# Kernel optimization log

Measured on AMD Instinct MI355X. Metric: run time of the kernel, lower is better.

Reference implementation:

```python
import jax, jax.numpy as jnp
import numpy as np

B, S, I, H, C, V = 512, 64, 300, 1024, 2, 50000


def setup_inputs() -> dict:
    key = jax.random.key(0)
    ks = jax.random.split(key, 10)
    s = 0.05
    return {
        "x": jax.random.randint(ks[0], (B, S), 0, V),
        "lengths": jax.random.randint(ks[1], (B,), 1, S + 1),
        "embed": jax.random.normal(ks[2], (V, I), jnp.float32) * s,
        "Wih_e": jax.random.normal(ks[3], (4 * H, I), jnp.float32) * s,
        "Whh_e": jax.random.normal(ks[4], (4 * H, H), jnp.float32) * s,
        "bih_e": jnp.zeros((4 * H,), jnp.float32),
        "bhh_e": jnp.zeros((4 * H,), jnp.float32),
        "Wih_d": jax.random.normal(ks[5], (4 * H, I), jnp.float32) * s,
        "Whh_d": jax.random.normal(ks[6], (4 * H, H), jnp.float32) * s,
        "bih_d": jnp.zeros((4 * H,), jnp.float32),
        "bhh_d": jnp.zeros((4 * H,), jnp.float32),
        "W_lin": jax.random.normal(ks[7], (C, H), jnp.float32) * s,
        "b_lin": jnp.zeros((C,), jnp.float32),
    }


def lstm_cell(xi, h, c, Wih, Whh, bih, bhh):
    # PyTorch LSTMCell gate order: i, f, g, o
    g = xi @ Wih.T + bih + h @ Whh.T + bhh
    i, f, gg, o = jnp.split(g, 4, axis=-1)
    c = jax.nn.sigmoid(f) * c + jax.nn.sigmoid(i) * jnp.tanh(gg)
    return jax.nn.sigmoid(o) * jnp.tanh(c), c


def reference(x, lengths, embed, Wih_e, Whh_e, bih_e, bhh_e,
              Wih_d, Whh_d, bih_d, bhh_d, W_lin, b_lin):
    bsz, slen = x.shape
    hdim = Whh_e.shape[1]
    ncls = W_lin.shape[0]
    xs = embed[x.T]                      # [S, B, I] (seq-major, like x.transpose(0,1))

    h0 = jnp.zeros((bsz, hdim), xs.dtype)
    c0 = jnp.zeros((bsz, hdim), xs.dtype)

    def enc_step(carry, xi):
        h, c = carry
        h, c = lstm_cell(xi, h, c, Wih_e, Whh_e, bih_e, bhh_e)
        return (h, c), h

    # forward pass over sequence
    (h, c), enc_fwd = jax.lax.scan(enc_step, (h0, c0), xs)          # enc_fwd: [S,B,H]
    # backward pass with the SAME encoder cell, continuing from (h, c)
    (h, c), h_bwd = jax.lax.scan(enc_step, (h, c), xs[::-1])        # h_bwd:  [S,B,H]
    # k-th backward step pairs with encoder_forward[k] in the original code
    enc_out = (enc_fwd + h_bwd) * 0.5                               # [S,B,H]

    def dec_step(carry, xi):
        h, c = carry
        # original attention sums over batch AND hidden -> one scalar per timestep,
        # and rebuilds w as a fresh Variable (no gradient through the weights).
        w = jax.nn.softmax(jnp.sum(h[None, :, :] * enc_out, axis=(1, 2)))  # [S]
        w = jax.lax.stop_gradient(w)
        h = h + jnp.einsum('t,tbh->bh', w, enc_out)
        h, c = lstm_cell(xi, h, c, Wih_d, Whh_d, bih_d, bhh_d)
        return (h, c), h

    _, dec = jax.lax.scan(dec_step, (h, c), xs)                     # [S,B,H]

    out = dec @ W_lin.T + b_lin                                     # [S,B,C]
    out = out.transpose(1, 0, 2)                                    # [B,S,C]
    pad = jnp.array([1.0, 0.0], out.dtype)                          # overwrite beyond lengths
    mask = jnp.arange(slen)[None, :] < lengths[:, None]             # [B,S]
    out = jnp.where(mask[:, :, None], out, pad)
    return out.reshape(bsz * slen, ncls)
```

## Files before the change

### kernel.cpp

```cpp
#include <hip/hip_runtime.h>
#include <hip/hip_bf16.h>

#define BSZ 512
#define SEQ 64
#define IDIM 300
#define KP1 384
#define HDIM 1024
#define G4 4096
#define BH (BSZ*HDIM)

typedef __attribute__((ext_vector_type(8))) short bf16x8;
typedef __attribute__((ext_vector_type(4))) float f32x4;
typedef __attribute__((ext_vector_type(8))) unsigned short u16x8;
typedef __attribute__((ext_vector_type(4))) unsigned short u16x4;

__device__ __forceinline__ float sigmoidf_(float x){ return 1.f/(1.f+__expf(-x)); }
__device__ __forceinline__ float bf2f(unsigned short u){
    union{unsigned int i; float f;} v; v.i = ((unsigned)u)<<16; return v.f;
}
__device__ __forceinline__ unsigned short f2bf(float f){
    __hip_bfloat16 b = __float2bfloat16(f);
    return *(unsigned short*)&b;
}

__global__ void embed_gather_k(const int* __restrict__ x, const float* __restrict__ embed,
                               __hip_bfloat16* __restrict__ xs){
    int t = blockIdx.x, b = blockIdx.y;
    int ix = x[b*SEQ + t];
    const float* src = embed + (size_t)ix * IDIM;
    __hip_bfloat16* dst = xs + ((size_t)t*BSZ + b) * KP1;
    for (int k = threadIdx.x; k < KP1; k += 64)
        dst[k] = __float2bfloat16(k < IDIM ? src[k] : 0.f);
}

__global__ void conv_w_k(const float* __restrict__ Wih_e, const float* __restrict__ Wih_d,
                         const float* __restrict__ Whh_e, const float* __restrict__ Whh_d,
                         __hip_bfloat16* __restrict__ Pe, __hip_bfloat16* __restrict__ Pd,
                         __hip_bfloat16* __restrict__ He, __hip_bfloat16* __restrict__ Hd){
    int nr = blockIdx.x, v = blockIdx.y;
    int orig = ((nr>>5)&3)*HDIM + (nr>>7)*32 + (nr&31);
    if (v < 2){
        const float* src = (v ? Wih_d : Wih_e) + (size_t)orig*IDIM;
        __hip_bfloat16* dst = (v ? Pd : Pe) + (size_t)nr*KP1;
        for (int k = threadIdx.x; k < KP1; k += 64)
            dst[k] = __float2bfloat16(k < IDIM ? src[k] : 0.f);
    } else {
        const float* src = ((v == 3) ? Whh_d : Whh_e) + (size_t)orig*HDIM;
        __hip_bfloat16* dst = ((v == 3) ? Hd : He) + (size_t)nr*HDIM;
        for (int k = threadIdx.x; k < HDIM; k += 64)
            dst[k] = __float2bfloat16(src[k]);
    }
}

__global__ void bias_comb_k(const float* __restrict__ a, const float* __restrict__ b2,
                            const float* __restrict__ c2, const float* __restrict__ d2,
                            float* __restrict__ be, float* __restrict__ bd){
    int i = blockIdx.x*256 + threadIdx.x;
    int nr = i & 4095;
    int orig = ((nr>>5)&3)*HDIM + (nr>>7)*32 + (nr&31);
    if (i < G4) be[nr] = a[orig] + b2[orig];
    else        bd[nr] = c2[orig] + d2[orig];
}

__global__ void zero_hc_k(float* __restrict__ h, float* __restrict__ c,
                          __hip_bfloat16* __restrict__ h_bf){
    int idx = blockIdx.x*256 + threadIdx.x;
    h[idx] = 0.f; c[idx] = 0.f; h_bf[idx] = __float2bfloat16(0.f);
}

#define BM 64
#define BN 128
#define NK1 (KP1/128)
#define NK2 (HDIM/128)
#define NKT (NK1+NK2)

__global__ __launch_bounds__(512) void lstm_step_k(
    const __hip_bfloat16* __restrict__ A1, const __hip_bfloat16* __restrict__ B1,
    const __hip_bfloat16* __restrict__ A2, const __hip_bfloat16* __restrict__ B2,
    const float* __restrict__ bias,
    float* __restrict__ c, float* __restrict__ h, __hip_bfloat16* __restrict__ h_bf,
    __hip_bfloat16* __restrict__ encSlot, int mode)
{
    __shared__ __align__(16) char smem[98304];
    const int tid  = threadIdx.x;
    const int lane = tid & 63, wv = tid >> 6;
    const int row0 = blockIdx.y * BM;
    const int col0 = blockIdx.x * BN;
    const int wm = wv >> 2, wn = wv & 3;

    f32x4 acc[2][2] = {};

    auto stage = [&](int ks, int p){
        const __hip_bfloat16* A; const __hip_bfloat16* B; int KA, k0;
        if (ks < NK1){ A = A1; B = B1; KA = KP1;  k0 = ks*128; }
        else         { A = A2; B = B2; KA = HDIM; k0 = (ks-NK1)*128; }
        char* base = smem + p*49152;
        #pragma unroll
        for (int half = 0; half < 2; ++half){
            int u = half*512 + tid;
            int r = u >> 4, s = u & 15;
            int g = s ^ (r & 15);
            const __hip_bfloat16* src = A + (size_t)(row0 + r)*KA + k0 + g*8;
            char* dst = base + half*8192 + wv*1024;
            __builtin_amdgcn_global_load_lds(
                (const __attribute__((address_space(1))) void*)src,
                (__attribute__((address_space(3))) void*)dst, 16, 0, 0);
        }
        #pragma unroll
        for (int q = 0; q < 4; ++q){
            int u = q*512 + tid;
            int r = u >> 4, s = u & 15;
            int g = s ^ (r & 15);
            const __hip_bfloat16* src = B + (size_t)(col0 + r)*KA + k0 + g*8;
            char* dst = base + 16384 + q*8192 + wv*1024;
            __builtin_amdgcn_global_load_lds(
                (const __attribute__((address_space(1))) void*)src,
                (__attribute__((address_space(3))) void*)dst, 16, 0, 0);
        }
    };

    auto compute = [&](int p){
        const char* Ab = smem + p*49152;
        const char* Bb = Ab + 16384;
        const int rr = lane & 15, g = lane >> 4;
        bf16x8 af[2][4], bfr[2][4];
        #pragma unroll
        for (int m = 0; m < 2; ++m){
            int r = wm*32 + m*16 + rr;
            #pragma unroll
            for (int kk = 0; kk < 4; ++kk)
                af[m][kk] = *(const bf16x8*)(Ab + r*256 + ((kk*4 + g) ^ (r & 15))*16);
        }
        #pragma unroll
        for (int n = 0; n < 2; ++n){
            int r = wn*32 + n*16 + rr;
            #pragma unroll
            for (int kk = 0; kk < 4; ++kk)
                bfr[n][kk] = *(const bf16x8*)(Bb + r*256 + ((kk*4 + g) ^ (r & 15))*16);
        }
        #pragma unroll
        for (int kk = 0; kk < 4; ++kk)
            #pragma unroll
            for (int m = 0; m < 2; ++m)
                #pragma unroll
                for (int n = 0; n < 2; ++n)
                    acc[m][n] = __builtin_amdgcn_mfma_f32_16x16x32_bf16(af[m][kk], bfr[n][kk], acc[m][n], 0, 0, 0);
    };

    const int erow = tid >> 3;
    const int ejj0 = (tid & 7) * 4;
    const size_t ebase = (size_t)(row0 + erow)*HDIM + blockIdx.x*32 + ejj0;

    stage(0, 0);
    const f32x4 cpre = *(const f32x4*)(c + ebase);
    __syncthreads();
    for (int ks = 0; ks < NKT; ++ks){
        int p = ks & 1;
        if (ks + 1 < NKT) stage(ks + 1, p ^ 1);
        compute(p);
        __syncthreads();
    }

    float* ep = (float*)smem;
    {
        const int rr = lane & 15, q4 = lane >> 4;
        #pragma unroll
        for (int m = 0; m < 2; ++m){
            int row = wm*32 + m*16 + q4*4;
            #pragma unroll
            for (int n = 0; n < 2; ++n){
                int jj = n*16 + rr;
                float bi = bias[col0 + wn*32 + jj];
                #pragma unroll
                for (int q = 0; q < 4; ++q)
                    ep[(wn*64 + row + q)*33 + jj] = acc[m][n][q] + bi;
            }
        }
    }
    __syncthreads();
    {
        f32x4 cv, hv;
        #pragma unroll
        for (int e = 0; e < 4; ++e){
            float gi = ep[(0*64 + erow)*33 + ejj0 + e];
            float gf = ep[(1*64 + erow)*33 + ejj0 + e];
            float gg = ep[(2*64 + erow)*33 + ejj0 + e];
            float go = ep[(3*64 + erow)*33 + ejj0 + e];
            float cc = sigmoidf_(gf)*cpre[e] + sigmoidf_(gi)*tanhf(gg);
            float hh = sigmoidf_(go)*tanhf(cc);
            cv[e] = cc; hv[e] = hh;
        }
        *(f32x4*)(c + ebase) = cv;
        *(f32x4*)(h + ebase) = hv;
        u16x4 hb;
        #pragma unroll
        for (int e = 0; e < 4; ++e) hb[e] = f2bf(hv[e]);
        *(u16x4*)(h_bf + ebase) = hb;
        if (mode == 0){
            *(u16x4*)(encSlot + ebase) = hb;
        } else if (mode == 1){
            u16x4 eo = *(const u16x4*)(encSlot + ebase);
            u16x4 r;
            #pragma unroll
            for (int e = 0; e < 4; ++e) r[e] = f2bf(0.5f*(bf2f(eo[e]) + hv[e]));
            *(u16x4*)(encSlot + ebase) = r;
        }
    }
}

__global__ __launch_bounds__(256) void attn_part_k(
    const __hip_bfloat16* __restrict__ h_bf, const __hip_bfloat16* __restrict__ enc,
    float* __restrict__ part,
    const float* __restrict__ h, const float* __restrict__ Wl, const float* __restrict__ bl,
    const int* __restrict__ len, float* __restrict__ out, int dect)
{
    __shared__ float red[4];
    int lane = threadIdx.x & 63, w = threadIdx.x >> 6;
    if (blockIdx.x < 64){
        int ch = blockIdx.x;
        int s  = blockIdx.y;
        const u16x8* e  = (const u16x8*)(enc + (size_t)s*BH + (size_t)ch*8192);
        const u16x8* hp = (const u16x8*)(h_bf + (size_t)ch*8192);
        float sum = 0.f;
        for (int i = threadIdx.x; i < 1024; i += 256){
            u16x8 ev = e[i], hv = hp[i];
            #pragma unroll
            for (int j = 0; j < 8; ++j) sum += bf2f(hv[j]) * bf2f(ev[j]);
        }
        #pragma unroll
        for (int m = 32; m >= 1; m >>= 1) sum += __shfl_xor(sum, m);
        if (lane == 0) red[w] = sum;
        __syncthreads();
        if (threadIdx.x == 0) part[s*64 + ch] = red[0]+red[1]+red[2]+red[3];
    } else if (dect >= 0){
        int b = ((blockIdx.x - 64)*64 + blockIdx.y)*4 + w;
        const float* hb = h + (size_t)b*HDIM;
        float s0 = 0.f, s1 = 0.f;
        for (int j = lane; j < HDIM; j += 64){
            float v = hb[j];
            s0 += v * Wl[j];
            s1 += v * Wl[HDIM + j];
        }
        #pragma unroll
        for (int m = 32; m >= 1; m >>= 1){ s0 += __shfl_xor(s0, m); s1 += __shfl_xor(s1, m); }
        if (lane == 0){
            bool valid = dect < len[b];
            size_t r = ((size_t)b*SEQ + dect)*2;
            out[r]   = valid ? (s0 + bl[0]) : 1.0f;
            out[r+1] = valid ? (s1 + bl[1]) : 0.0f;
        }
    }
}

__global__ __launch_bounds__(256) void attn_apply_k(
    const float* __restrict__ h, const float* __restrict__ part,
    const __hip_bfloat16* __restrict__ enc, __hip_bfloat16* __restrict__ hat_bf)
{
    __shared__ float wl[64];
    int lane = threadIdx.x & 63;
    if (threadIdx.x < 64){
        float tot = 0.f;
        #pragma unroll 8
        for (int ch = 0; ch < 64; ++ch) tot += part[lane*64 + ch];
        float m = tot;
        #pragma unroll
        for (int msk = 32; msk >= 1; msk >>= 1) m = fmaxf(m, __shfl_xor(m, msk));
        float e = __expf(tot - m);
        float sm = e;
        #pragma unroll
        for (int msk = 32; msk >= 1; msk >>= 1) sm += __shfl_xor(sm, msk);
        wl[lane] = e / sm;
    }
    __syncthreads();
    size_t i4 = ((size_t)blockIdx.x*256 + threadIdx.x) * 4;
    float v[4];
    {
        f32x4 a = *(const f32x4*)(h + i4);
        v[0]=a[0]; v[1]=a[1]; v[2]=a[2]; v[3]=a[3];
    }
    for (int s = 0; s < SEQ; ++s){
        u16x4 ev = *(const u16x4*)(enc + (size_t)s*BH + i4);
        float w = wl[s];
        #pragma unroll
        for (int j = 0; j < 4; ++j) v[j] += w * bf2f(ev[j]);
    }
    u16x4 ov;
    #pragma unroll
    for (int j = 0; j < 4; ++j) ov[j] = f2bf(v[j]);
    *(u16x4*)(hat_bf + i4) = ov;
}

__global__ void dec_linear_k(const float* __restrict__ h, const float* __restrict__ Wl,
                             const float* __restrict__ bl, const int* __restrict__ len,
                             float* __restrict__ out, int t)
{
    int b = blockIdx.x, lane = threadIdx.x;
    const float* hb = h + (size_t)b*HDIM;
    float s0 = 0.f, s1 = 0.f;
    for (int j = lane; j < HDIM; j += 64){
        float v = hb[j];
        s0 += v * Wl[j];
        s1 += v * Wl[HDIM + j];
    }
    #pragma unroll
    for (int m = 32; m >= 1; m >>= 1){ s0 += __shfl_xor(s0, m); s1 += __shfl_xor(s1, m); }
    if (lane == 0){
        bool valid = t < len[b];
        size_t r = ((size_t)b*SEQ + t)*2;
        out[r]   = valid ? (s0 + bl[0]) : 1.0f;
        out[r+1] = valid ? (s1 + bl[1]) : 0.0f;
    }
}

extern "C" void kernel_launch(void* const* d_in, const int* in_sizes, int n_in,
                              void* d_out, int out_size, void* d_ws, size_t ws_size,
                              hipStream_t stream)
{
    (void)in_sizes; (void)n_in; (void)out_size; (void)ws_size;
    const int*   x      = (const int*)  d_in[0];
    const int*   len    = (const int*)  d_in[1];
    const float* embed  = (const float*)d_in[2];
    const float* Wih_e  = (const float*)d_in[3];
    const float* Whh_e  = (const float*)d_in[4];
    const float* bih_e  = (const float*)d_in[5];
    const float* bhh_e  = (const float*)d_in[6];
    const float* Wih_d  = (const float*)d_in[7];
    const float* Whh_d  = (const float*)d_in[8];
    const float* bih_d  = (const float*)d_in[9];
    const float* bhh_d  = (const float*)d_in[10];
    const float* W_lin  = (const float*)d_in[11];
    const float* b_lin  = (const float*)d_in[12];
    float* out = (float*)d_out;

    float* ws = (float*)d_ws;
    size_t off = 0;
    auto alloc = [&](size_t nfloats){ size_t o = off; off += (nfloats + 63) & ~(size_t)63; return o; };
    __hip_bfloat16* xs_bf  = (__hip_bfloat16*)(ws + alloc((size_t)SEQ*BSZ*KP1/2));
    __hip_bfloat16* Pe     = (__hip_bfloat16*)(ws + alloc((size_t)G4*KP1/2));
    __hip_bfloat16* Pd     = (__hip_bfloat16*)(ws + alloc((size_t)G4*KP1/2));
    __hip_bfloat16* He     = (__hip_bfloat16*)(ws + alloc((size_t)G4*HDIM/2));
    __hip_bfloat16* Hd     = (__hip_bfloat16*)(ws + alloc((size_t)G4*HDIM/2));
    float* be   = ws + alloc(G4);
    float* bd   = ws + alloc(G4);
    float* h    = ws + alloc(BH);
    float* c    = ws + alloc(BH);
    __hip_bfloat16* h_bf   = (__hip_bfloat16*)(ws + alloc(BH/2));
    __hip_bfloat16* hat_bf = (__hip_bfloat16*)(ws + alloc(BH/2));
    __hip_bfloat16* enc    = (__hip_bfloat16*)(ws + alloc((size_t)SEQ*BH/2));
    float* part = ws + alloc(64*64);

    embed_gather_k<<<dim3(SEQ, BSZ), 64, 0, stream>>>(x, embed, xs_bf);
    conv_w_k<<<dim3(G4, 4), 64, 0, stream>>>(Wih_e, Wih_d, Whh_e, Whh_d, Pe, Pd, He, Hd);
    bias_comb_k<<<32, 256, 0, stream>>>(bih_e, bhh_e, bih_d, bhh_d, be, bd);
    zero_hc_k<<<BH/256, 256, 0, stream>>>(h, c, h_bf);

    dim3 ggrid(G4/BN, BSZ/BM);

    for (int t = 0; t < SEQ; ++t)
        lstm_step_k<<<ggrid, 512, 0, stream>>>(xs_bf + (size_t)t*BSZ*KP1, Pe, h_bf, He, be,
                                               c, h, h_bf, enc + (size_t)t*BH, 0);
    for (int k = 0; k < SEQ; ++k)
        lstm_step_k<<<ggrid, 512, 0, stream>>>(xs_bf + (size_t)(SEQ-1-k)*BSZ*KP1, Pe, h_bf, He, be,
                                               c, h, h_bf, enc + (size_t)k*BH, 1);
    for (int t = 0; t < SEQ; ++t){
        attn_part_k<<<dim3(66, 64), 256, 0, stream>>>(h_bf, enc, part, h, W_lin, b_lin, len, out, t - 1);
        attn_apply_k<<<512, 256, 0, stream>>>(h, part, enc, hat_bf);
        lstm_step_k<<<ggrid, 512, 0, stream>>>(xs_bf + (size_t)t*BSZ*KP1, Pd, hat_bf, Hd, bd,
                                               c, h, h_bf, nullptr, 2);
    }
    dec_linear_k<<<BSZ, 64, 0, stream>>>(h, W_lin, b_lin, len, out, SEQ - 1);
}
```

Baseline: 4.348 ms.

## Use 4-wave LSTM GEMM blocks with larger per-wave tiles and batch attention scores

The LSTM step GEMM now runs 256 threads (4 waves) per block instead of 512, and each wave computes a 32x64 output tile with 8 MFMA accumulators. This raises fragment reuse per LDS read but halves the waves available for latency hiding. The gate epilogue is remapped so each thread handles 8 contiguous columns with wider vector stores. Separately, the attention score kernel keeps h in registers and reuses it across 8 timesteps per block, which cuts repeated h loads and shrinks the grid from 66x64 to 640 blocks.

```diff
diff --git a/kernel.cpp b/kernel.cpp
--- a/kernel.cpp
+++ b/kernel.cpp
@@ -74,7 +74,7 @@
 #define NK2 (HDIM/128)
 #define NKT (NK1+NK2)
 
-__global__ __launch_bounds__(512) void lstm_step_k(
+__global__ __launch_bounds__(256) void lstm_step_k(
     const __hip_bfloat16* __restrict__ A1, const __hip_bfloat16* __restrict__ B1,
     const __hip_bfloat16* __restrict__ A2, const __hip_bfloat16* __restrict__ B2,
     const float* __restrict__ bias,
@@ -86,9 +86,9 @@
     const int lane = tid & 63, wv = tid >> 6;
     const int row0 = blockIdx.y * BM;
     const int col0 = blockIdx.x * BN;
-    const int wm = wv >> 2, wn = wv & 3;
-
-    f32x4 acc[2][2] = {};
+    const int wm = wv >> 1, wn = wv & 1;
+
+    f32x4 acc[2][4] = {};
 
     auto stage = [&](int ks, int p){
         const __hip_bfloat16* A; const __hip_bfloat16* B; int KA, k0;
@@ -96,23 +96,23 @@
         else         { A = A2; B = B2; KA = HDIM; k0 = (ks-NK1)*128; }
         char* base = smem + p*49152;
         #pragma unroll
-        for (int half = 0; half < 2; ++half){
-            int u = half*512 + tid;
+        for (int q = 0; q < 4; ++q){
+            int u = q*256 + tid;
             int r = u >> 4, s = u & 15;
             int g = s ^ (r & 15);
             const __hip_bfloat16* src = A + (size_t)(row0 + r)*KA + k0 + g*8;
-            char* dst = base + half*8192 + wv*1024;
+            char* dst = base + q*4096 + wv*1024;
             __builtin_amdgcn_global_load_lds(
                 (const __attribute__((address_space(1))) void*)src,
                 (__attribute__((address_space(3))) void*)dst, 16, 0, 0);
         }
         #pragma unroll
-        for (int q = 0; q < 4; ++q){
-            int u = q*512 + tid;
+        for (int q = 0; q < 8; ++q){
+            int u = q*256 + tid;
             int r = u >> 4, s = u & 15;
             int g = s ^ (r & 15);
             const __hip_bfloat16* src = B + (size_t)(col0 + r)*KA + k0 + g*8;
-            char* dst = base + 16384 + q*8192 + wv*1024;
+            char* dst = base + 16384 + q*4096 + wv*1024;
             __builtin_amdgcn_global_load_lds(
                 (const __attribute__((address_space(1))) void*)src,
                 (__attribute__((address_space(3))) void*)dst, 16, 0, 0);
@@ -123,7 +123,7 @@
         const char* Ab = smem + p*49152;
         const char* Bb = Ab + 16384;
         const int rr = lane & 15, g = lane >> 4;
-        bf16x8 af[2][4], bfr[2][4];
+        bf16x8 af[2][4], bfr[4][4];
         #pragma unroll
         for (int m = 0; m < 2; ++m){
             int r = wm*32 + m*16 + rr;
@@ -132,8 +132,8 @@
                 af[m][kk] = *(const bf16x8*)(Ab + r*256 + ((kk*4 + g) ^ (r & 15))*16);
         }
         #pragma unroll
-        for (int n = 0; n < 2; ++n){
-            int r = wn*32 + n*16 + rr;
+        for (int n = 0; n < 4; ++n){
+            int r = wn*64 + n*16 + rr;
             #pragma unroll
             for (int kk = 0; kk < 4; ++kk)
                 bfr[n][kk] = *(const bf16x8*)(Bb + r*256 + ((kk*4 + g) ^ (r & 15))*16);
@@ -143,16 +143,17 @@
             #pragma unroll
             for (int m = 0; m < 2; ++m)
                 #pragma unroll
-                for (int n = 0; n < 2; ++n)
+                for (int n = 0; n < 4; ++n)
                     acc[m][n] = __builtin_amdgcn_mfma_f32_16x16x32_bf16(af[m][kk], bfr[n][kk], acc[m][n], 0, 0, 0);
     };
 
-    const int erow = tid >> 3;
-    const int ejj0 = (tid & 7) * 4;
+    const int erow = tid >> 2;
+    const int ejj0 = (tid & 3) * 8;
     const size_t ebase = (size_t)(row0 + erow)*HDIM + blockIdx.x*32 + ejj0;
 
     stage(0, 0);
-    const f32x4 cpre = *(const f32x4*)(c + ebase);
+    const f32x4 cpre0 = *(const f32x4*)(c + ebase);
+    const f32x4 cpre1 = *(const f32x4*)(c + ebase + 4);
     __syncthreads();
     for (int ks = 0; ks < NKT; ++ks){
         int p = ks & 1;
@@ -168,42 +169,46 @@
         for (int m = 0; m < 2; ++m){
             int row = wm*32 + m*16 + q4*4;
             #pragma unroll
-            for (int n = 0; n < 2; ++n){
-                int jj = n*16 + rr;
-                float bi = bias[col0 + wn*32 + jj];
+            for (int n = 0; n < 4; ++n){
+                int cib = wn*64 + n*16 + rr;
+                int gate = cib >> 5, jj = cib & 31;
+                float bi = bias[col0 + cib];
                 #pragma unroll
                 for (int q = 0; q < 4; ++q)
-                    ep[(wn*64 + row + q)*33 + jj] = acc[m][n][q] + bi;
+                    ep[(gate*64 + row + q)*33 + jj] = acc[m][n][q] + bi;
             }
         }
     }
     __syncthreads();
     {
-        f32x4 cv, hv;
-        #pragma unroll
-        for (int e = 0; e < 4; ++e){
+        f32x4 cv0, cv1, hv0, hv1;
+        float hvf[8];
+        #pragma unroll
+        for (int e = 0; e < 8; ++e){
             float gi = ep[(0*64 + erow)*33 + ejj0 + e];
             float gf = ep[(1*64 + erow)*33 + ejj0 + e];
             float gg = ep[(2*64 + erow)*33 + ejj0 + e];
             float go = ep[(3*64 + erow)*33 + ejj0 + e];
-            float cc = sigmoidf_(gf)*cpre[e] + sigmoidf_(gi)*tanhf(gg);
+            float cp = (e < 4) ? cpre0[e] : cpre1[e-4];
+            float cc = sigmoidf_(gf)*cp + sigmoidf_(gi)*tanhf(gg);
             float hh = sigmoidf_(go)*tanhf(cc);
-            cv[e] = cc; hv[e] = hh;
-        }
-        *(f32x4*)(c + ebase) = cv;
-        *(f32x4*)(h + ebase) = hv;
-        u16x4 hb;
-        #pragma unroll
-        for (int e = 0; e < 4; ++e) hb[e] = f2bf(hv[e]);
-        *(u16x4*)(h_bf + ebase) = hb;
+            if (e < 4){ cv0[e] = cc; hv0[e] = hh; } else { cv1[e-4] = cc; hv1[e-4] = hh; }
+            hvf[e] = hh;
+        }
+        *(f32x4*)(c + ebase) = cv0; *(f32x4*)(c + ebase + 4) = cv1;
+        *(f32x4*)(h + ebase) = hv0; *(f32x4*)(h + ebase + 4) = hv1;
+        u16x8 hb;
+        #pragma unroll
+        for (int e = 0; e < 8; ++e) hb[e] = f2bf(hvf[e]);
+        *(u16x8*)(h_bf + ebase) = hb;
         if (mode == 0){
-            *(u16x4*)(encSlot + ebase) = hb;
+            *(u16x8*)(encSlot + ebase) = hb;
         } else if (mode == 1){
-            u16x4 eo = *(const u16x4*)(encSlot + ebase);
-            u16x4 r;
-            #pragma unroll
-            for (int e = 0; e < 4; ++e) r[e] = f2bf(0.5f*(bf2f(eo[e]) + hv[e]));
-            *(u16x4*)(encSlot + ebase) = r;
+            u16x8 eo = *(const u16x8*)(encSlot + ebase);
+            u16x8 r;
+            #pragma unroll
+            for (int e = 0; e < 8; ++e) r[e] = f2bf(0.5f*(bf2f(eo[e]) + hvf[e]));
+            *(u16x8*)(encSlot + ebase) = r;
         }
     }
 }
@@ -214,26 +219,39 @@
     const float* __restrict__ h, const float* __restrict__ Wl, const float* __restrict__ bl,
     const int* __restrict__ len, float* __restrict__ out, int dect)
 {
-    __shared__ float red[4];
     int lane = threadIdx.x & 63, w = threadIdx.x >> 6;
-    if (blockIdx.x < 64){
-        int ch = blockIdx.x;
-        int s  = blockIdx.y;
-        const u16x8* e  = (const u16x8*)(enc + (size_t)s*BH + (size_t)ch*8192);
+    if (blockIdx.x < 512){
+        int ch = blockIdx.x & 63;
+        int s0 = (blockIdx.x >> 6) * 8;
         const u16x8* hp = (const u16x8*)(h_bf + (size_t)ch*8192);
-        float sum = 0.f;
-        for (int i = threadIdx.x; i < 1024; i += 256){
-            u16x8 ev = e[i], hv = hp[i];
-            #pragma unroll
-            for (int j = 0; j < 8; ++j) sum += bf2f(hv[j]) * bf2f(ev[j]);
-        }
-        #pragma unroll
-        for (int m = 32; m >= 1; m >>= 1) sum += __shfl_xor(sum, m);
-        if (lane == 0) red[w] = sum;
+        float hf[4][8];
+        #pragma unroll
+        for (int k = 0; k < 4; ++k){
+            u16x8 hv = hp[threadIdx.x + k*256];
+            #pragma unroll
+            for (int j = 0; j < 8; ++j) hf[k][j] = bf2f(hv[j]);
+        }
+        __shared__ float red[8][4];
+        for (int si = 0; si < 8; ++si){
+            const u16x8* e = (const u16x8*)(enc + (size_t)(s0 + si)*BH + (size_t)ch*8192);
+            float sum = 0.f;
+            #pragma unroll
+            for (int k = 0; k < 4; ++k){
+                u16x8 ev = e[threadIdx.x + k*256];
+                #pragma unroll
+                for (int j = 0; j < 8; ++j) sum += hf[k][j] * bf2f(ev[j]);
+            }
+            #pragma unroll
+            for (int m = 32; m >= 1; m >>= 1) sum += __shfl_xor(sum, m);
+            if (lane == 0) red[si][w] = sum;
+        }
         __syncthreads();
-        if (threadIdx.x == 0) part[s*64 + ch] = red[0]+red[1]+red[2]+red[3];
+        if (threadIdx.x < 8){
+            int si = threadIdx.x;
+            part[(s0 + si)*64 + ch] = red[si][0]+red[si][1]+red[si][2]+red[si][3];
+        }
     } else if (dect >= 0){
-        int b = ((blockIdx.x - 64)*64 + blockIdx.y)*4 + w;
+        int b = (blockIdx.x - 512)*4 + w;
         const float* hb = h + (size_t)b*HDIM;
         float s0 = 0.f, s1 = 0.f;
         for (int j = lane; j < HDIM; j += 64){
@@ -357,15 +375,15 @@
     dim3 ggrid(G4/BN, BSZ/BM);
 
     for (int t = 0; t < SEQ; ++t)
-        lstm_step_k<<<ggrid, 512, 0, stream>>>(xs_bf + (size_t)t*BSZ*KP1, Pe, h_bf, He, be,
+        lstm_step_k<<<ggrid, 256, 0, stream>>>(xs_bf + (size_t)t*BSZ*KP1, Pe, h_bf, He, be,
                                                c, h, h_bf, enc + (size_t)t*BH, 0);
     for (int k = 0; k < SEQ; ++k)
-        lstm_step_k<<<ggrid, 512, 0, stream>>>(xs_bf + (size_t)(SEQ-1-k)*BSZ*KP1, Pe, h_bf, He, be,
+        lstm_step_k<<<ggrid, 256, 0, stream>>>(xs_bf + (size_t)(SEQ-1-k)*BSZ*KP1, Pe, h_bf, He, be,
                                                c, h, h_bf, enc + (size_t)k*BH, 1);
     for (int t = 0; t < SEQ; ++t){
-        attn_part_k<<<dim3(66, 64), 256, 0, stream>>>(h_bf, enc, part, h, W_lin, b_lin, len, out, t - 1);
+        attn_part_k<<<640, 256, 0, stream>>>(h_bf, enc, part, h, W_lin, b_lin, len, out, t - 1);
         attn_apply_k<<<512, 256, 0, stream>>>(h, part, enc, hat_bf);
-        lstm_step_k<<<ggrid, 512, 0, stream>>>(xs_bf + (size_t)t*BSZ*KP1, Pd, hat_bf, Hd, bd,
+        lstm_step_k<<<ggrid, 256, 0, stream>>>(xs_bf + (size_t)t*BSZ*KP1, Pd, hat_bf, Hd, bd,
                                                c, h, h_bf, nullptr, 2);
     }
     dec_linear_k<<<BSZ, 64, 0, stream>>>(h, W_lin, b_lin, len, out, SEQ - 1);
```

After: 4.394 ms. No clear change (+1.1%).

## Precompute encoder input projections once and reuse them in forward and backward passes

Applied to the files above, without the earlier changes.

Adds a kernel that computes the x @ Wih_e^T products for all timesteps once and stores them in a fp32 workspace laid out in per-thread accumulator order. The encoder step kernel, templated on XPRE, starts its accumulators from these stored values and runs only the recurrent Whh K-loop. This removes the repeated input GEMM from the 128 encoder steps, since the forward and backward passes share the same input projection. The cost is a large extra workspace buffer (about 537 MB) with a fallback to the old path when the workspace is too small, plus extra per-step global reads of the stored accumulators.

```diff
diff --git a/kernel.cpp b/kernel.cpp
--- a/kernel.cpp
+++ b/kernel.cpp
@@ -74,13 +74,108 @@
 #define NK2 (HDIM/128)
 #define NKT (NK1+NK2)
 
+__global__ __launch_bounds__(512) void xpre_k(
+    const __hip_bfloat16* __restrict__ xs, const __hip_bfloat16* __restrict__ B1,
+    float* __restrict__ Gx)
+{
+    __shared__ __align__(16) char smem[131072];
+    const int tid  = threadIdx.x;
+    const int lane = tid & 63, wv = tid >> 6;
+    const int row0 = blockIdx.y * BM;
+    const int col0 = blockIdx.x * BN;
+    const int wm = wv >> 2, wn = wv & 3;
+    const int fb = blockIdx.y*32 + blockIdx.x;
+
+    #pragma unroll
+    for (int ks = 0; ks < 3; ++ks)
+        #pragma unroll
+        for (int q = 0; q < 4; ++q){
+            int u = q*512 + tid;
+            int r = u >> 4, s = u & 15;
+            int g = s ^ (r & 15);
+            const __hip_bfloat16* src = B1 + (size_t)(col0 + r)*KP1 + ks*128 + g*8;
+            char* dst = smem + ks*32768 + q*8192 + wv*1024;
+            __builtin_amdgcn_global_load_lds(
+                (const __attribute__((address_space(1))) void*)src,
+                (__attribute__((address_space(3))) void*)dst, 16, 0, 0);
+        }
+
+    auto stage_a = [&](int t, int ks, int p){
+        #pragma unroll
+        for (int half = 0; half < 2; ++half){
+            int u = half*512 + tid;
+            int r = u >> 4, s = u & 15;
+            int g = s ^ (r & 15);
+            const __hip_bfloat16* src = xs + (size_t)t*BSZ*KP1 + (size_t)(row0 + r)*KP1 + ks*128 + g*8;
+            char* dst = smem + 98304 + p*16384 + half*8192 + wv*1024;
+            __builtin_amdgcn_global_load_lds(
+                (const __attribute__((address_space(1))) void*)src,
+                (__attribute__((address_space(3))) void*)dst, 16, 0, 0);
+        }
+    };
+
+    f32x4 acc[2][2] = {};
+    auto compute_a = [&](int p, int ks){
+        const char* Ab = smem + 98304 + p*16384;
+        const char* Bb = smem + ks*32768;
+        const int rr = lane & 15, g = lane >> 4;
+        bf16x8 af[2][4], bfr[2][4];
+        #pragma unroll
+        for (int m = 0; m < 2; ++m){
+            int r = wm*32 + m*16 + rr;
+            #pragma unroll
+            for (int kk = 0; kk < 4; ++kk)
+                af[m][kk] = *(const bf16x8*)(Ab + r*256 + ((kk*4 + g) ^ (r & 15))*16);
+        }
+        #pragma unroll
+        for (int n = 0; n < 2; ++n){
+            int r = wn*32 + n*16 + rr;
+            #pragma unroll
+            for (int kk = 0; kk < 4; ++kk)
+                bfr[n][kk] = *(const bf16x8*)(Bb + r*256 + ((kk*4 + g) ^ (r & 15))*16);
+        }
+        #pragma unroll
+        for (int kk = 0; kk < 4; ++kk)
+            #pragma unroll
+            for (int m = 0; m < 2; ++m)
+                #pragma unroll
+                for (int n = 0; n < 2; ++n)
+                    acc[m][n] = __builtin_amdgcn_mfma_f32_16x16x32_bf16(af[m][kk], bfr[n][kk], acc[m][n], 0, 0, 0);
+    };
+
+    stage_a(0, 0, 0);
+    __syncthreads();
+    for (int t = 0; t < SEQ; ++t){
+        #pragma unroll
+        for (int ks = 0; ks < 3; ++ks){
+            int u = t*3 + ks;
+            int p = u & 1;
+            if (u + 1 < SEQ*3) stage_a((u+1)/3, (u+1)%3, p ^ 1);
+            compute_a(p, ks);
+            if (ks == 2){
+                float* gp = Gx + (((size_t)t*256 + fb)*512 + tid)*16;
+                #pragma unroll
+                for (int m = 0; m < 2; ++m)
+                    #pragma unroll
+                    for (int n = 0; n < 2; ++n)
+                        *(f32x4*)(gp + (m*2+n)*4) = acc[m][n];
+                acc[0][0] = f32x4{}; acc[0][1] = f32x4{};
+                acc[1][0] = f32x4{}; acc[1][1] = f32x4{};
+            }
+            __syncthreads();
+        }
+    }
+}
+
+template<int XPRE>
 __global__ __launch_bounds__(512) void lstm_step_k(
     const __hip_bfloat16* __restrict__ A1, const __hip_bfloat16* __restrict__ B1,
     const __hip_bfloat16* __restrict__ A2, const __hip_bfloat16* __restrict__ B2,
-    const float* __restrict__ bias,
+    const float* __restrict__ bias, const float* __restrict__ Gxt,
     float* __restrict__ c, float* __restrict__ h, __hip_bfloat16* __restrict__ h_bf,
     __hip_bfloat16* __restrict__ encSlot, int mode)
 {
+    constexpr int NKT_ = XPRE ? NK2 : NKT;
     __shared__ __align__(16) char smem[98304];
     const int tid  = threadIdx.x;
     const int lane = tid & 63, wv = tid >> 6;
@@ -88,12 +183,26 @@
     const int col0 = blockIdx.x * BN;
     const int wm = wv >> 2, wn = wv & 3;
 
-    f32x4 acc[2][2] = {};
+    f32x4 acc[2][2];
+    if constexpr (XPRE){
+        const float* gp = Gxt + (((size_t)(blockIdx.y*32 + blockIdx.x))*512 + tid)*16;
+        #pragma unroll
+        for (int m = 0; m < 2; ++m)
+            #pragma unroll
+            for (int n = 0; n < 2; ++n)
+                acc[m][n] = *(const f32x4*)(gp + (m*2+n)*4);
+    } else {
+        acc[0][0] = f32x4{}; acc[0][1] = f32x4{};
+        acc[1][0] = f32x4{}; acc[1][1] = f32x4{};
+    }
 
     auto stage = [&](int ks, int p){
         const __hip_bfloat16* A; const __hip_bfloat16* B; int KA, k0;
-        if (ks < NK1){ A = A1; B = B1; KA = KP1;  k0 = ks*128; }
-        else         { A = A2; B = B2; KA = HDIM; k0 = (ks-NK1)*128; }
+        if constexpr (XPRE){ A = A2; B = B2; KA = HDIM; k0 = ks*128; }
+        else {
+            if (ks < NK1){ A = A1; B = B1; KA = KP1;  k0 = ks*128; }
+            else         { A = A2; B = B2; KA = HDIM; k0 = (ks-NK1)*128; }
+        }
         char* base = smem + p*49152;
         #pragma unroll
         for (int half = 0; half < 2; ++half){
@@ -154,9 +263,9 @@
     stage(0, 0);
     const f32x4 cpre = *(const f32x4*)(c + ebase);
     __syncthreads();
-    for (int ks = 0; ks < NKT; ++ks){
+    for (int ks = 0; ks < NKT_; ++ks){
         int p = ks & 1;
-        if (ks + 1 < NKT) stage(ks + 1, p ^ 1);
+        if (ks + 1 < NKT_) stage(ks + 1, p ^ 1);
         compute(p);
         __syncthreads();
     }
@@ -316,7 +425,7 @@
                               void* d_out, int out_size, void* d_ws, size_t ws_size,
                               hipStream_t stream)
 {
-    (void)in_sizes; (void)n_in; (void)out_size; (void)ws_size;
+    (void)in_sizes; (void)n_in; (void)out_size;
     const int*   x      = (const int*)  d_in[0];
     const int*   len    = (const int*)  d_in[1];
     const float* embed  = (const float*)d_in[2];
@@ -348,25 +457,43 @@
     __hip_bfloat16* hat_bf = (__hip_bfloat16*)(ws + alloc(BH/2));
     __hip_bfloat16* enc    = (__hip_bfloat16*)(ws + alloc((size_t)SEQ*BH/2));
     float* part = ws + alloc(64*64);
+    float* Gx   = ws + alloc((size_t)SEQ*256*512*16);
+    const bool useGx = (off * sizeof(float)) <= ws_size;
 
     embed_gather_k<<<dim3(SEQ, BSZ), 64, 0, stream>>>(x, embed, xs_bf);
     conv_w_k<<<dim3(G4, 4), 64, 0, stream>>>(Wih_e, Wih_d, Whh_e, Whh_d, Pe, Pd, He, Hd);
     bias_comb_k<<<32, 256, 0, stream>>>(bih_e, bhh_e, bih_d, bhh_d, be, bd);
     zero_hc_k<<<BH/256, 256, 0, stream>>>(h, c, h_bf);
+    if (useGx)
+        xpre_k<<<dim3(32, 8), 512, 0, stream>>>(xs_bf, Pe, Gx);
 
     dim3 ggrid(G4/BN, BSZ/BM);
-
-    for (int t = 0; t < SEQ; ++t)
-        lstm_step_k<<<ggrid, 512, 0, stream>>>(xs_bf + (size_t)t*BSZ*KP1, Pe, h_bf, He, be,
-                                               c, h, h_bf, enc + (size_t)t*BH, 0);
-    for (int k = 0; k < SEQ; ++k)
-        lstm_step_k<<<ggrid, 512, 0, stream>>>(xs_bf + (size_t)(SEQ-1-k)*BSZ*KP1, Pe, h_bf, He, be,
-                                               c, h, h_bf, enc + (size_t)k*BH, 1);
+    const size_t gxstep = (size_t)256*512*16;
+
+    for (int t = 0; t < SEQ; ++t){
+        if (useGx)
+            lstm_step_k<1><<<ggrid, 512, 0, stream>>>(xs_bf + (size_t)t*BSZ*KP1, Pe, h_bf, He, be,
+                                                      Gx + (size_t)t*gxstep,
+                                                      c, h, h_bf, enc + (size_t)t*BH, 0);
+        else
+            lstm_step_k<0><<<ggrid, 512, 0, stream>>>(xs_bf + (size_t)t*BSZ*KP1, Pe, h_bf, He, be,
+                                                      nullptr, c, h, h_bf, enc + (size_t)t*BH, 0);
+    }
+    for (int k = 0; k < SEQ; ++k){
+        int t = SEQ - 1 - k;
+        if (useGx)
+            lstm_step_k<1><<<ggrid, 512, 0, stream>>>(xs_bf + (size_t)t*BSZ*KP1, Pe, h_bf, He, be,
+                                                      Gx + (size_t)t*gxstep,
+                                                      c, h, h_bf, enc + (size_t)k*BH, 1);
+        else
+            lstm_step_k<0><<<ggrid, 512, 0, stream>>>(xs_bf + (size_t)t*BSZ*KP1, Pe, h_bf, He, be,
+                                                      nullptr, c, h, h_bf, enc + (size_t)k*BH, 1);
+    }
     for (int t = 0; t < SEQ; ++t){
         attn_part_k<<<dim3(66, 64), 256, 0, stream>>>(h_bf, enc, part, h, W_lin, b_lin, len, out, t - 1);
         attn_apply_k<<<512, 256, 0, stream>>>(h, part, enc, hat_bf);
-        lstm_step_k<<<ggrid, 512, 0, stream>>>(xs_bf + (size_t)t*BSZ*KP1, Pd, hat_bf, Hd, bd,
-                                               c, h, h_bf, nullptr, 2);
+        lstm_step_k<0><<<ggrid, 512, 0, stream>>>(xs_bf + (size_t)t*BSZ*KP1, Pd, hat_bf, Hd, bd,
+                                                  nullptr, c, h, h_bf, nullptr, 2);
     }
     dec_linear_k<<<BSZ, 64, 0, stream>>>(h, W_lin, b_lin, len, out, SEQ - 1);
 }
```

New measurement: 4.336 ms. About the same (-0.3%).
